# Kernel tuning notes

Hardware: AMD Instinct MI355X
Metric: run time of the kernel (lower is better)

The kernel has to match this reference:

```python
import jax, jax.numpy as jnp
import numpy as np

EMB = 1024
NH = 16
HS = EMB // NH

def setup_inputs() -> dict:
    key = jax.random.key(0)
    ks = jax.random.split(key, 9)
    s = 0.02
    x = jax.random.normal(ks[0], (4, 2048, EMB), dtype=jnp.float32)
    Wq = jax.random.normal(ks[1], (EMB, EMB), dtype=jnp.float32) * s
    bq = jnp.zeros((EMB,), jnp.float32)
    Wk = jax.random.normal(ks[2], (EMB, EMB), dtype=jnp.float32) * s
    bk = jnp.zeros((EMB,), jnp.float32)
    Wv = jax.random.normal(ks[3], (EMB, EMB), dtype=jnp.float32) * s
    bv = jnp.zeros((EMB,), jnp.float32)
    Wo = jax.random.normal(ks[4], (EMB, EMB), dtype=jnp.float32) * s
    bo = jnp.zeros((EMB,), jnp.float32)
    return {"x": x, "Wq": Wq, "bq": bq, "Wk": Wk, "bk": bk,
            "Wv": Wv, "bv": bv, "Wo": Wo, "bo": bo}

def reference(x, Wq, bq, Wk, bk, Wv, bv, Wo, bo):
    B, T, C = x.shape
    q = x @ Wq + bq
    k = x @ Wk + bk
    v = x @ Wv + bv
    # [B, H, T, hs]
    q = q.reshape(B, T, NH, HS).transpose(0, 2, 1, 3)
    k = k.reshape(B, T, NH, HS).transpose(0, 2, 1, 3)
    v = v.reshape(B, T, NH, HS).transpose(0, 2, 1, 3)
    scale = 1.0 / np.sqrt(HS).astype(np.float32)
    att = jnp.einsum('bhqd,bhkd->bhqk', q, k) * scale
    causal = jnp.tril(jnp.ones((T, T), dtype=bool))
    att = jnp.where(causal[None, None], att, jnp.float32(-jnp.inf))
    att = jax.nn.softmax(att, axis=-1)
    y = jnp.einsum('bhqk,bhkd->bhqd', att, v)
    y = y.transpose(0, 2, 1, 3).reshape(B, T, C)
    return y @ Wo + bo
```

## Files before the change

kernel.cpp:

```cpp
#include <hip/hip_runtime.h>

#define EMB   1024
#define NHEAD 16
#define HS    64
#define BATCH 4
#define SEQ   2048
#define MTOK  (BATCH*SEQ)

typedef __bf16 bf16;
typedef __bf16 bf16x8 __attribute__((ext_vector_type(8)));
typedef __bf16 bf16x4 __attribute__((ext_vector_type(4)));
typedef float  f32x4  __attribute__((ext_vector_type(4)));
typedef _Float16 f16;
typedef f16 f16x4 __attribute__((ext_vector_type(4)));
typedef f16 f16x8 __attribute__((ext_vector_type(8)));

#define MFMA16(a,b,c)     __builtin_amdgcn_mfma_f32_16x16x32_bf16(a,b,c,0,0,0)
#define MFMA_H32(a,b,c)   __builtin_amdgcn_mfma_f32_16x16x32_f16(a,b,c,0,0,0)
#define MFMA_H16(a,b,c)   __builtin_amdgcn_mfma_f32_16x16x16f16(a,b,c,0,0,0)

#if __has_builtin(__builtin_amdgcn_exp2f)
#define EXP2(x) __builtin_amdgcn_exp2f(x)
#else
#define EXP2(x) exp2f(x)
#endif

#define GLL(g, l) __builtin_amdgcn_global_load_lds(                         \
        (const __attribute__((address_space(1))) void*)(g),                 \
        (__attribute__((address_space(3))) void*)(l), 16, 0, 0)

__global__ __launch_bounds__(256) void k_convert_x(const float* __restrict__ x,
                                                   bf16* __restrict__ xb) {
    int i = (blockIdx.x * 256 + threadIdx.x) * 4;
    float4 v = *(const float4*)(x + i);
    bf16x4 o;
    o[0] = (bf16)v.x; o[1] = (bf16)v.y; o[2] = (bf16)v.z; o[3] = (bf16)v.w;
    *(bf16x4*)(xb + i) = o;
}

__global__ __launch_bounds__(256) void k_transpose_w4(
        const float* __restrict__ W0, const float* __restrict__ W1,
        const float* __restrict__ W2, const float* __restrict__ W3,
        bf16* __restrict__ T0, bf16* __restrict__ T1,
        bf16* __restrict__ T2, bf16* __restrict__ T3) {
    __shared__ float tile[64][65];
    const int z = blockIdx.z;
    const float* W = (z == 0) ? W0 : (z == 1) ? W1 : (z == 2) ? W2 : W3;
    bf16* Wt = (z == 0) ? T0 : (z == 1) ? T1 : (z == 2) ? T2 : T3;
    int c0 = blockIdx.x * 64, r0 = blockIdx.y * 64;
    int tx = threadIdx.x & 63, ty = threadIdx.x >> 6;
    #pragma unroll
    for (int r = ty; r < 64; r += 4)
        tile[r][tx] = W[(r0 + r) * EMB + c0 + tx];
    __syncthreads();
    #pragma unroll
    for (int cc = ty; cc < 64; cc += 4)
        Wt[(c0 + cc) * EMB + r0 + tx] = (bf16)tile[tx][cc];
}

__global__ __launch_bounds__(256) void k_qkv_gemm(
        const bf16* __restrict__ xb,
        const bf16* __restrict__ Wqt, const bf16* __restrict__ Wkt, const bf16* __restrict__ Wvt,
        const float* __restrict__ bq, const float* __restrict__ bk, const float* __restrict__ bv,
        f16* __restrict__ Q, f16* __restrict__ K, f16* __restrict__ Vt) {
    __shared__ __align__(16) bf16 As[128 * 32];
    __shared__ __align__(16) bf16 Bs[128 * 32];
    const int tid = threadIdx.x;
    const int lane = tid & 63;
    const int wave = tid >> 6;
    const int l15 = lane & 15, quad = lane >> 4;
    const int wm = (wave >> 1) * 64, wn = (wave & 1) * 64;
    const int m0 = blockIdx.x * 128;
    const int gy = blockIdx.y;
    const int which = gy >> 3;
    const int n0 = (gy & 7) * 128;
    const bf16* Wt  = (which == 0) ? Wqt : (which == 1) ? Wkt : Wvt;
    const float* bias = (which == 0) ? bq : (which == 1) ? bk : bv;

    f32x4 acc[4][4];
    #pragma unroll
    for (int i = 0; i < 4; i++)
        #pragma unroll
        for (int j = 0; j < 4; j++) acc[i][j] = (f32x4){0.f, 0.f, 0.f, 0.f};

    const int srow = tid >> 2, skc = (tid & 3) * 8;
    const bf16* Ag = xb + (size_t)m0 * EMB + srow * EMB + skc;
    const bf16* Bg = Wt + (size_t)n0 * EMB + srow * EMB + skc;

    for (int k0 = 0; k0 < EMB; k0 += 32) {
        __syncthreads();
        GLL(Ag + k0,            As + tid * 8);
        GLL(Ag + 64 * EMB + k0, As + (tid + 256) * 8);
        GLL(Bg + k0,            Bs + tid * 8);
        GLL(Bg + 64 * EMB + k0, Bs + (tid + 256) * 8);
        __syncthreads();

        bf16x8 af[4], bfr[4];
        #pragma unroll
        for (int rf = 0; rf < 4; rf++)
            af[rf] = *(const bf16x8*)(As + (wm + rf * 16 + l15) * 32 + quad * 8);
        #pragma unroll
        for (int cf = 0; cf < 4; cf++)
            bfr[cf] = *(const bf16x8*)(Bs + (wn + cf * 16 + l15) * 32 + quad * 8);
        #pragma unroll
        for (int rf = 0; rf < 4; rf++)
            #pragma unroll
            for (int cf = 0; cf < 4; cf++)
                acc[rf][cf] = MFMA16(af[rf], bfr[cf], acc[rf][cf]);
    }

    const float QSCALE = 0.18033688011112043f;
    #pragma unroll
    for (int cf = 0; cf < 4; cf++) {
        const int col = n0 + wn + cf * 16 + l15;
        const float bv_ = bias[col];
        const int h = col >> 6, d = col & 63;
        #pragma unroll
        for (int rf = 0; rf < 4; rf++) {
            #pragma unroll
            for (int r = 0; r < 4; r++) {
                const int row = m0 + wm + rf * 16 + quad * 4 + r;
                const int b_ = row >> 11, t = row & (SEQ - 1);
                const float val = acc[rf][cf][r] + bv_;
                if (which == 0) {
                    Q[((size_t)(b_ * NHEAD + h) * SEQ + t) * HS + d] = (f16)(val * QSCALE);
                } else if (which == 1) {
                    K[((size_t)(b_ * NHEAD + h) * SEQ + t) * HS + d] = (f16)val;
                } else {
                    Vt[(((size_t)(b_ * NHEAD + h) * 32 + (t >> 6)) * 64 + d) * 64 + (t & 63)] = (f16)val;
                }
            }
        }
    }
}

__global__ __launch_bounds__(256) void k_attn(
        const f16* __restrict__ Q, const f16* __restrict__ K,
        const f16* __restrict__ Vt, bf16* __restrict__ y) {
    __shared__ __align__(16) f16 kbuf[2][64 * 64];
    __shared__ __align__(16) f16 vbuf[2][64 * 64];
    const int tid = threadIdx.x;
    const int wave = tid >> 6, lane = tid & 63;
    const int l15 = lane & 15, quad = lane >> 4;
    const int qtA = blockIdx.x;
    const int bh = blockIdx.y;
    const int h = bh & (NHEAD - 1), b_ = bh >> 4;

    const f16* Qb = Q + (size_t)bh * SEQ * HS;
    const f16* Kb = K + (size_t)bh * SEQ * HS;
    const f16* Vb = Vt + (size_t)bh * 32 * 4096;

    const int c0 = tid, c1 = tid + 256;
    const int soff0 = (c0 >> 3) * 64 + (((c0 & 7) ^ ((c0 >> 3) & 7)) * 8);
    const int soff1 = (c1 >> 3) * 64 + (((c1 & 7) ^ ((c1 >> 3) & 7)) * 8);
    const int swz = l15 & 7;

    f16x4 ones;
    #pragma unroll
    for (int i = 0; i < 4; i++) ones[i] = (f16)1.0f;

    #pragma unroll 1
    for (int phase = 0; phase < 2; ++phase) {
        const int qt = phase ? (15 - qtA) : qtA;
        const int ntiles = 2 * qt + 2;
        const int qrow0 = qt * 128 + wave * 32;

        f16x8 qb[2][2];
        #pragma unroll
        for (int qf = 0; qf < 2; qf++)
            #pragma unroll
            for (int dk = 0; dk < 2; dk++)
                qb[qf][dk] = *(const f16x8*)(Qb + (qrow0 + 16 * qf + l15) * HS + 32 * dk + quad * 8);

        f32x4 o[2][4], lacc[2];
        #pragma unroll
        for (int qf = 0; qf < 2; qf++) {
            lacc[qf] = (f32x4){0.f, 0.f, 0.f, 0.f};
            #pragma unroll
            for (int df = 0; df < 4; df++) o[qf][df] = (f32x4){0.f, 0.f, 0.f, 0.f};
        }

        f16x8 kr0 = *(const f16x8*)(Kb + c0 * 8);
        f16x8 kr1 = *(const f16x8*)(Kb + c1 * 8);
        f16x8 vr0 = *(const f16x8*)(Vb + c0 * 8);
        f16x8 vr1 = *(const f16x8*)(Vb + c1 * 8);
        __syncthreads();
        *(f16x8*)(kbuf[0] + soff0) = kr0;
        *(f16x8*)(kbuf[0] + soff1) = kr1;
        *(f16x8*)(vbuf[0] + soff0) = vr0;
        *(f16x8*)(vbuf[0] + soff1) = vr1;

        for (int it = 0; it < ntiles; ++it) {
            const int kv0 = it * 64;
            __syncthreads();
            if (it + 1 < ntiles) {
                const f16* kg = Kb + (size_t)(kv0 + 64) * HS;
                const f16* vg = Vb + (size_t)(it + 1) * 4096;
                kr0 = *(const f16x8*)(kg + c0 * 8);
                kr1 = *(const f16x8*)(kg + c1 * 8);
                vr0 = *(const f16x8*)(vg + c0 * 8);
                vr1 = *(const f16x8*)(vg + c1 * 8);
            }
            if (kv0 <= qrow0 + 31) {
                const f16* kb_ = kbuf[it & 1];
                const f16* vb_ = vbuf[it & 1];

                f32x4 s[4][2];
                #pragma unroll
                for (int mb = 0; mb < 4; mb++) {
                    f16x8 ka0 = *(const f16x8*)(kb_ + (16 * mb + l15) * 64 + ((quad ^ swz) * 8));
                    f16x8 ka1 = *(const f16x8*)(kb_ + (16 * mb + l15) * 64 + (((4 + quad) ^ swz) * 8));
                    #pragma unroll
                    for (int qf = 0; qf < 2; qf++) {
                        f32x4 t = (f32x4){0.f, 0.f, 0.f, 0.f};
                        t = MFMA_H32(ka0, qb[qf][0], t);
                        t = MFMA_H32(ka1, qb[qf][1], t);
                        s[mb][qf] = t;
                    }
                }

                f16x4 pa[4][2];
                const bool edge = (kv0 + 63 > qrow0);
                #pragma unroll
                for (int mb = 0; mb < 4; mb++)
                    #pragma unroll
                    for (int qf = 0; qf < 2; qf++) {
                        f16x4 p;
                        if (edge) {
                            #pragma unroll
                            for (int r = 0; r < 4; r++) {
                                const int kvc = kv0 + 16 * mb + quad * 4 + r;
                                const int qq  = qrow0 + 16 * qf + l15;
                                p[r] = (f16)((kvc <= qq) ? EXP2(s[mb][qf][r]) : 0.f);
                            }
                        } else {
                            #pragma unroll
                            for (int r = 0; r < 4; r++)
                                p[r] = (f16)EXP2(s[mb][qf][r]);
                        }
                        pa[mb][qf] = p;
                    }

                #pragma unroll
                for (int df = 0; df < 4; df++)
                    #pragma unroll
                    for (int kb = 0; kb < 4; kb++) {
                        f16x4 vfrag = *(const f16x4*)(vb_ + (16 * df + l15) * 64 +
                                        (((2 * kb + (quad >> 1)) ^ swz) * 8) + (quad & 1) * 4);
                        #pragma unroll
                        for (int qf = 0; qf < 2; qf++)
                            o[qf][df] = MFMA_H16(pa[kb][qf], vfrag, o[qf][df]);
                    }
                #pragma unroll
                for (int kb = 0; kb < 4; kb++)
                    #pragma unroll
                    for (int qf = 0; qf < 2; qf++)
                        lacc[qf] = MFMA_H16(pa[kb][qf], ones, lacc[qf]);
            }
            if (it + 1 < ntiles) {
                const int nb = (it + 1) & 1;
                *(f16x8*)(kbuf[nb] + soff0) = kr0;
                *(f16x8*)(kbuf[nb] + soff1) = kr1;
                *(f16x8*)(vbuf[nb] + soff0) = vr0;
                *(f16x8*)(vbuf[nb] + soff1) = vr1;
            }
        }

        #pragma unroll
        for (int qf = 0; qf < 2; qf++)
            #pragma unroll
            for (int r = 0; r < 4; r++) {
                float inv = 1.f / lacc[qf][r];
                int t = qrow0 + 16 * qf + quad * 4 + r;
                bf16* yp = y + ((size_t)(b_ * SEQ + t)) * EMB + h * HS;
                #pragma unroll
                for (int df = 0; df < 4; df++)
                    yp[df * 16 + l15] = (bf16)(o[qf][df][r] * inv);
            }
    }
}

__global__ __launch_bounds__(256) void k_out_gemm(
        const bf16* __restrict__ y, const bf16* __restrict__ Wot,
        const float* __restrict__ bo, float* __restrict__ out) {
    __shared__ __align__(16) bf16 As[128 * 32];
    __shared__ __align__(16) bf16 Bs[128 * 32];
    const int tid = threadIdx.x;
    const int lane = tid & 63;
    const int wave = tid >> 6;
    const int l15 = lane & 15, quad = lane >> 4;
    const int wm = (wave >> 1) * 64, wn = (wave & 1) * 64;
    const int m0 = blockIdx.x * 128;
    const int n0 = blockIdx.y * 128;

    f32x4 acc[4][4];
    #pragma unroll
    for (int i = 0; i < 4; i++)
        #pragma unroll
        for (int j = 0; j < 4; j++) acc[i][j] = (f32x4){0.f, 0.f, 0.f, 0.f};

    const int srow = tid >> 2, skc = (tid & 3) * 8;
    const bf16* Ag = y  + (size_t)m0 * EMB + srow * EMB + skc;
    const bf16* Bg = Wot + (size_t)n0 * EMB + srow * EMB + skc;

    for (int k0 = 0; k0 < EMB; k0 += 32) {
        __syncthreads();
        GLL(Ag + k0,            As + tid * 8);
        GLL(Ag + 64 * EMB + k0, As + (tid + 256) * 8);
        GLL(Bg + k0,            Bs + tid * 8);
        GLL(Bg + 64 * EMB + k0, Bs + (tid + 256) * 8);
        __syncthreads();

        bf16x8 af[4], bfr[4];
        #pragma unroll
        for (int rf = 0; rf < 4; rf++)
            af[rf] = *(const bf16x8*)(As + (wm + rf * 16 + l15) * 32 + quad * 8);
        #pragma unroll
        for (int cf = 0; cf < 4; cf++)
            bfr[cf] = *(const bf16x8*)(Bs + (wn + cf * 16 + l15) * 32 + quad * 8);
        #pragma unroll
        for (int rf = 0; rf < 4; rf++)
            #pragma unroll
            for (int cf = 0; cf < 4; cf++)
                acc[rf][cf] = MFMA16(af[rf], bfr[cf], acc[rf][cf]);
    }

    #pragma unroll
    for (int cf = 0; cf < 4; cf++) {
        const int col = n0 + wn + cf * 16 + l15;
        const float bv_ = bo[col];
        #pragma unroll
        for (int rf = 0; rf < 4; rf++) {
            #pragma unroll
            for (int r = 0; r < 4; r++) {
                const int row = m0 + wm + rf * 16 + quad * 4 + r;
                out[(size_t)row * EMB + col] = acc[rf][cf][r] + bv_;
            }
        }
    }
}

extern "C" void kernel_launch(void* const* d_in, const int* in_sizes, int n_in,
                              void* d_out, int out_size, void* d_ws, size_t ws_size,
                              hipStream_t stream) {
    const float* x  = (const float*)d_in[0];
    const float* Wq = (const float*)d_in[1];
    const float* bq = (const float*)d_in[2];
    const float* Wk = (const float*)d_in[3];
    const float* bk = (const float*)d_in[4];
    const float* Wv = (const float*)d_in[5];
    const float* bv = (const float*)d_in[6];
    const float* Wo = (const float*)d_in[7];
    const float* bo = (const float*)d_in[8];
    float* out = (float*)d_out;

    char* ws = (char*)d_ws;
    bf16* xb  = (bf16*)(ws);
    bf16* Wqt = (bf16*)(ws + (16u << 20));
    bf16* Wkt = (bf16*)(ws + (18u << 20));
    bf16* Wvt = (bf16*)(ws + (20u << 20));
    bf16* Wot = (bf16*)(ws + (22u << 20));
    f16*  Q   = (f16*)(ws + (24u << 20));
    f16*  K   = (f16*)(ws + (40u << 20));
    f16*  Vt  = (f16*)(ws + (56u << 20));
    bf16* y   = (bf16*)(ws + (72u << 20));

    k_convert_x<<<(MTOK * EMB) / (256 * 4), 256, 0, stream>>>(x, xb);
    dim3 tg(EMB / 64, EMB / 64, 4);
    k_transpose_w4<<<tg, 256, 0, stream>>>(Wq, Wk, Wv, Wo, Wqt, Wkt, Wvt, Wot);

    dim3 g1(MTOK / 128, 24);
    k_qkv_gemm<<<g1, 256, 0, stream>>>(xb, Wqt, Wkt, Wvt, bq, bk, bv, Q, K, Vt);

    dim3 g2(SEQ / 256, BATCH * NHEAD);
    k_attn<<<g2, 256, 0, stream>>>(Q, K, Vt, y);

    dim3 g3(MTOK / 128, EMB / 128);
    k_out_gemm<<<g3, 256, 0, stream>>>(y, Wot, bo, out);
}
```

Measured before the change: 293.9 us.

## Double GEMM K-tile with XOR-swizzled LDS and merge prep kernels

Both the QKV and output GEMMs now stage 64-wide K tiles instead of 32, halving the number of barrier-separated load phases. The LDS layout uses an XOR swizzle on 16-byte chunks to avoid bank conflicts on the fragment reads. The x conversion and the weight transposes are merged into one launch to save a kernel launch. In exchange, LDS use per block doubles and more fragment registers are live, which may lower occupancy.

Result: no change. 289.7 us (-1.4%).

```diff
diff --git a/kernel.cpp b/kernel.cpp
--- a/kernel.cpp
+++ b/kernel.cpp
@@ -29,24 +29,28 @@
         (const __attribute__((address_space(1))) void*)(g),                 \
         (__attribute__((address_space(3))) void*)(l), 16, 0, 0)
 
-__global__ __launch_bounds__(256) void k_convert_x(const float* __restrict__ x,
-                                                   bf16* __restrict__ xb) {
-    int i = (blockIdx.x * 256 + threadIdx.x) * 4;
-    float4 v = *(const float4*)(x + i);
-    bf16x4 o;
-    o[0] = (bf16)v.x; o[1] = (bf16)v.y; o[2] = (bf16)v.z; o[3] = (bf16)v.w;
-    *(bf16x4*)(xb + i) = o;
-}
-
-__global__ __launch_bounds__(256) void k_transpose_w4(
+__global__ __launch_bounds__(256) void k_prep(
+        const float* __restrict__ x, bf16* __restrict__ xb,
         const float* __restrict__ W0, const float* __restrict__ W1,
         const float* __restrict__ W2, const float* __restrict__ W3,
         bf16* __restrict__ T0, bf16* __restrict__ T1,
         bf16* __restrict__ T2, bf16* __restrict__ T3) {
+    const int z = blockIdx.z;
+    if (z == 0) {
+        const int blk = blockIdx.y * 16 + blockIdx.x;
+        const size_t base = (size_t)blk * 32768;
+        for (int j = threadIdx.x; j < 8192; j += 256) {
+            size_t i = base + (size_t)j * 4;
+            float4 v = *(const float4*)(x + i);
+            bf16x4 o;
+            o[0] = (bf16)v.x; o[1] = (bf16)v.y; o[2] = (bf16)v.z; o[3] = (bf16)v.w;
+            *(bf16x4*)(xb + i) = o;
+        }
+        return;
+    }
     __shared__ float tile[64][65];
-    const int z = blockIdx.z;
-    const float* W = (z == 0) ? W0 : (z == 1) ? W1 : (z == 2) ? W2 : W3;
-    bf16* Wt = (z == 0) ? T0 : (z == 1) ? T1 : (z == 2) ? T2 : T3;
+    const float* W = (z == 1) ? W0 : (z == 2) ? W1 : (z == 3) ? W2 : W3;
+    bf16* Wt = (z == 1) ? T0 : (z == 2) ? T1 : (z == 3) ? T2 : T3;
     int c0 = blockIdx.x * 64, r0 = blockIdx.y * 64;
     int tx = threadIdx.x & 63, ty = threadIdx.x >> 6;
     #pragma unroll
@@ -63,8 +67,8 @@
         const bf16* __restrict__ Wqt, const bf16* __restrict__ Wkt, const bf16* __restrict__ Wvt,
         const float* __restrict__ bq, const float* __restrict__ bk, const float* __restrict__ bv,
         f16* __restrict__ Q, f16* __restrict__ K, f16* __restrict__ Vt) {
-    __shared__ __align__(16) bf16 As[128 * 32];
-    __shared__ __align__(16) bf16 Bs[128 * 32];
+    __shared__ __align__(16) bf16 As[128 * 64];
+    __shared__ __align__(16) bf16 Bs[128 * 64];
     const int tid = threadIdx.x;
     const int lane = tid & 63;
     const int wave = tid >> 6;
@@ -83,30 +87,40 @@
         #pragma unroll
         for (int j = 0; j < 4; j++) acc[i][j] = (f32x4){0.f, 0.f, 0.f, 0.f};
 
-    const int srow = tid >> 2, skc = (tid & 3) * 8;
-    const bf16* Ag = xb + (size_t)m0 * EMB + srow * EMB + skc;
-    const bf16* Bg = Wt + (size_t)n0 * EMB + srow * EMB + skc;
-
-    for (int k0 = 0; k0 < EMB; k0 += 32) {
+    const int r0_ = tid >> 3;
+    const int kcs = ((tid & 7) ^ (r0_ & 7)) * 8;
+    const bf16* Ag = xb + (size_t)m0 * EMB + r0_ * EMB + kcs;
+    const bf16* Bg = Wt + (size_t)n0 * EMB + r0_ * EMB + kcs;
+    const int rsw = l15 & 7;
+
+    for (int k0 = 0; k0 < EMB; k0 += 64) {
         __syncthreads();
-        GLL(Ag + k0,            As + tid * 8);
-        GLL(Ag + 64 * EMB + k0, As + (tid + 256) * 8);
-        GLL(Bg + k0,            Bs + tid * 8);
-        GLL(Bg + 64 * EMB + k0, Bs + (tid + 256) * 8);
+        #pragma unroll
+        for (int g = 0; g < 4; g++) {
+            GLL(Ag + 32 * g * EMB + k0, As + (tid + g * 256) * 8);
+            GLL(Bg + 32 * g * EMB + k0, Bs + (tid + g * 256) * 8);
+        }
         __syncthreads();
 
-        bf16x8 af[4], bfr[4];
-        #pragma unroll
-        for (int rf = 0; rf < 4; rf++)
-            af[rf] = *(const bf16x8*)(As + (wm + rf * 16 + l15) * 32 + quad * 8);
-        #pragma unroll
-        for (int cf = 0; cf < 4; cf++)
-            bfr[cf] = *(const bf16x8*)(Bs + (wn + cf * 16 + l15) * 32 + quad * 8);
-        #pragma unroll
-        for (int rf = 0; rf < 4; rf++)
+        bf16x8 af[2][4], bfr[2][4];
+        #pragma unroll
+        for (int h = 0; h < 2; h++) {
+            #pragma unroll
+            for (int rf = 0; rf < 4; rf++)
+                af[h][rf] = *(const bf16x8*)(As + (wm + rf * 16 + l15) * 64 +
+                                             (((4 * h + quad) ^ rsw) * 8));
             #pragma unroll
             for (int cf = 0; cf < 4; cf++)
-                acc[rf][cf] = MFMA16(af[rf], bfr[cf], acc[rf][cf]);
+                bfr[h][cf] = *(const bf16x8*)(Bs + (wn + cf * 16 + l15) * 64 +
+                                              (((4 * h + quad) ^ rsw) * 8));
+        }
+        #pragma unroll
+        for (int h = 0; h < 2; h++)
+            #pragma unroll
+            for (int rf = 0; rf < 4; rf++)
+                #pragma unroll
+                for (int cf = 0; cf < 4; cf++)
+                    acc[rf][cf] = MFMA16(af[h][rf], bfr[h][cf], acc[rf][cf]);
     }
 
     const float QSCALE = 0.18033688011112043f;
@@ -283,8 +297,8 @@
 __global__ __launch_bounds__(256) void k_out_gemm(
         const bf16* __restrict__ y, const bf16* __restrict__ Wot,
         const float* __restrict__ bo, float* __restrict__ out) {
-    __shared__ __align__(16) bf16 As[128 * 32];
-    __shared__ __align__(16) bf16 Bs[128 * 32];
+    __shared__ __align__(16) bf16 As[128 * 64];
+    __shared__ __align__(16) bf16 Bs[128 * 64];
     const int tid = threadIdx.x;
     const int lane = tid & 63;
     const int wave = tid >> 6;
@@ -299,30 +313,40 @@
         #pragma unroll
         for (int j = 0; j < 4; j++) acc[i][j] = (f32x4){0.f, 0.f, 0.f, 0.f};
 
-    const int srow = tid >> 2, skc = (tid & 3) * 8;
-    const bf16* Ag = y  + (size_t)m0 * EMB + srow * EMB + skc;
-    const bf16* Bg = Wot + (size_t)n0 * EMB + srow * EMB + skc;
-
-    for (int k0 = 0; k0 < EMB; k0 += 32) {
+    const int r0_ = tid >> 3;
+    const int kcs = ((tid & 7) ^ (r0_ & 7)) * 8;
+    const bf16* Ag = y   + (size_t)m0 * EMB + r0_ * EMB + kcs;
+    const bf16* Bg = Wot + (size_t)n0 * EMB + r0_ * EMB + kcs;
+    const int rsw = l15 & 7;
+
+    for (int k0 = 0; k0 < EMB; k0 += 64) {
         __syncthreads();
-        GLL(Ag + k0,            As + tid * 8);
-        GLL(Ag + 64 * EMB + k0, As + (tid + 256) * 8);
-        GLL(Bg + k0,            Bs + tid * 8);
-        GLL(Bg + 64 * EMB + k0, Bs + (tid + 256) * 8);
+        #pragma unroll
+        for (int g = 0; g < 4; g++) {
+            GLL(Ag + 32 * g * EMB + k0, As + (tid + g * 256) * 8);
+            GLL(Bg + 32 * g * EMB + k0, Bs + (tid + g * 256) * 8);
+        }
         __syncthreads();
 
-        bf16x8 af[4], bfr[4];
-        #pragma unroll
-        for (int rf = 0; rf < 4; rf++)
-            af[rf] = *(const bf16x8*)(As + (wm + rf * 16 + l15) * 32 + quad * 8);
-        #pragma unroll
-        for (int cf = 0; cf < 4; cf++)
-            bfr[cf] = *(const bf16x8*)(Bs + (wn + cf * 16 + l15) * 32 + quad * 8);
-        #pragma unroll
-        for (int rf = 0; rf < 4; rf++)
+        bf16x8 af[2][4], bfr[2][4];
+        #pragma unroll
+        for (int h = 0; h < 2; h++) {
+            #pragma unroll
+            for (int rf = 0; rf < 4; rf++)
+                af[h][rf] = *(const bf16x8*)(As + (wm + rf * 16 + l15) * 64 +
+                                             (((4 * h + quad) ^ rsw) * 8));
             #pragma unroll
             for (int cf = 0; cf < 4; cf++)
-                acc[rf][cf] = MFMA16(af[rf], bfr[cf], acc[rf][cf]);
+                bfr[h][cf] = *(const bf16x8*)(Bs + (wn + cf * 16 + l15) * 64 +
+                                              (((4 * h + quad) ^ rsw) * 8));
+        }
+        #pragma unroll
+        for (int h = 0; h < 2; h++)
+            #pragma unroll
+            for (int rf = 0; rf < 4; rf++)
+                #pragma unroll
+                for (int cf = 0; cf < 4; cf++)
+                    acc[rf][cf] = MFMA16(af[h][rf], bfr[h][cf], acc[rf][cf]);
     }
 
     #pragma unroll
@@ -365,9 +389,8 @@
     f16*  Vt  = (f16*)(ws + (56u << 20));
     bf16* y   = (bf16*)(ws + (72u << 20));
 
-    k_convert_x<<<(MTOK * EMB) / (256 * 4), 256, 0, stream>>>(x, xb);
-    dim3 tg(EMB / 64, EMB / 64, 4);
-    k_transpose_w4<<<tg, 256, 0, stream>>>(Wq, Wk, Wv, Wo, Wqt, Wkt, Wvt, Wot);
+    dim3 gp(16, 16, 5);
+    k_prep<<<gp, 256, 0, stream>>>(x, xb, Wq, Wk, Wv, Wo, Wqt, Wkt, Wvt, Wot);
 
     dim3 g1(MTOK / 128, 24);
     k_qkv_gemm<<<g1, 256, 0, stream>>>(xb, Wqt, Wkt, Wvt, bq, bk, bv, Q, K, Vt);
```
